# Optimization experiments

Hardware: AMD Instinct MI355X
Metric: run time of the kernel (lower is better)

Reference implementation:

```python
import jax, jax.numpy as jnp
import numpy as np

EPS = 1e-5
CONV_THRESHOLD = 0.0


def setup_inputs() -> dict:
    key = jax.random.key(0)
    ks = jax.random.split(key, 16)
    B, F = 65536, 256
    H1, H2 = 1024, 512
    d_in = F + 1  # raw features + 1 scalar conv feature
    inp = {
        "x": jax.random.normal(ks[0], (B, F), dtype=jnp.float32),
        # layer 1: Linear(d_in, H1) + BatchNorm1d(H1)
        "W1": jax.random.normal(ks[1], (d_in, H1), dtype=jnp.float32) * (1.0 / np.sqrt(d_in)),
        "b1": jax.random.normal(ks[2], (H1,), dtype=jnp.float32) * 0.01,
        "g1": jnp.ones((H1,), jnp.float32) + 0.1 * jax.random.normal(ks[3], (H1,), dtype=jnp.float32),
        "be1": jax.random.normal(ks[4], (H1,), dtype=jnp.float32) * 0.01,
        "m1": jax.random.normal(ks[5], (H1,), dtype=jnp.float32) * 0.1,
        "v1": jax.random.uniform(ks[6], (H1,), dtype=jnp.float32, minval=0.5, maxval=1.5),
        # layer 2: Linear(H1, H2) + BatchNorm1d(H2)
        "W2": jax.random.normal(ks[7], (H1, H2), dtype=jnp.float32) * (1.0 / np.sqrt(H1)),
        "b2": jax.random.normal(ks[8], (H2,), dtype=jnp.float32) * 0.01,
        "g2": jnp.ones((H2,), jnp.float32) + 0.1 * jax.random.normal(ks[9], (H2,), dtype=jnp.float32),
        "be2": jax.random.normal(ks[10], (H2,), dtype=jnp.float32) * 0.01,
        "m2": jax.random.normal(ks[11], (H2,), dtype=jnp.float32) * 0.1,
        "v2": jax.random.uniform(ks[12], (H2,), dtype=jnp.float32, minval=0.5, maxval=1.5),
        # output head: Linear(H2, 1)
        "W3": jax.random.normal(ks[13], (H2, 1), dtype=jnp.float32) * (1.0 / np.sqrt(H2)),
        "b3": jax.random.normal(ks[14], (1,), dtype=jnp.float32) * 0.01,
    }
    return inp


def _bn(h, g, be, m, v):
    # eval-mode BatchNorm1d with running statistics
    return g * (h - m) * jax.lax.rsqrt(v + EPS) + be


def reference(x, W1, b1, g1, be1, m1, v1, W2, b2, g2, be2, m2, v2, W3, b3):
    # Batched replacement of the per-sample numpy threshold conv:
    # the Conv filter reduces the whole sample patch with a mean and thresholds it,
    # producing one binary scalar feature per sample.  [B, 1]
    conv_feat = jnp.where(jnp.mean(x, axis=1, keepdims=True) > CONV_THRESHOLD, 1.0, 0.0).astype(x.dtype)
    h = jnp.concatenate([x, conv_feat], axis=1)  # [B, F+1]
    h = jax.nn.relu(_bn(h @ W1 + b1, g1, be1, m1, v1))  # [B, H1]
    h = jax.nn.relu(_bn(h @ W2 + b2, g2, be2, m2, v2))  # [B, H2]
    return jax.nn.sigmoid(h @ W3 + b3)  # [B, 1]
```

## Files before the change

### kernel.cpp

```cpp
#include <hip/hip_runtime.h>
#include <hip/hip_bf16.h>
#include <cstdint>
#include <cstddef>

typedef __bf16 bf16_t;
typedef bf16_t bf16x8 __attribute__((ext_vector_type(8)));
typedef bf16_t bf16x4 __attribute__((ext_vector_type(4)));
typedef float f32x4 __attribute__((ext_vector_type(4)));

#define BN_EPS 1e-5f

__device__ __forceinline__ void async_load16(const bf16_t* g, bf16_t* lds) {
  __builtin_amdgcn_global_load_lds(
      (__attribute__((address_space(1))) uint32_t*)(g),
      (__attribute__((address_space(3))) uint32_t*)(lds),
      16, 0, 0);
}

__global__ void prep_all_kernel(const float* __restrict__ W1, const float* __restrict__ W2,
                                const float* b1, const float* g1, const float* be1,
                                const float* m1, const float* v1,
                                const float* b2, const float* g2, const float* be2,
                                const float* m2, const float* v2,
                                bf16_t* __restrict__ W1T, bf16_t* __restrict__ W2T,
                                float* s1, float* t1, float* s2, float* t2,
                                float* w1last) {
  const int b = blockIdx.x;
  if (b < 192) {
    const float* src;
    bf16_t* dst;
    int R, C, bx, by;
    if (b < 64) { src = W1; dst = W1T; R = 256; C = 1024; bx = b & 15; by = b >> 4; }
    else        { src = W2; dst = W2T; R = 1024; C = 512; bx = (b - 64) & 7; by = (b - 64) >> 3; }
    __shared__ bf16_t tile[64][66];
    const int r0 = by * 64, c0 = bx * 64;
    const int tc = threadIdx.x & 63;
    const int tr4 = threadIdx.x >> 6;
#pragma unroll
    for (int i = 0; i < 16; ++i) {
      int r = i * 4 + tr4;
      tile[r][tc] = (bf16_t)src[(size_t)(r0 + r) * C + c0 + tc];
    }
    __syncthreads();
#pragma unroll
    for (int i = 0; i < 16; ++i) {
      int rr = i * 4 + tr4;
      dst[(size_t)(c0 + rr) * R + r0 + tc] = tile[tc][rr];
    }
  } else {
    int i = (b - 192) * 256 + threadIdx.x;
    if (i < 1024) {
      float s = g1[i] * rsqrtf(v1[i] + BN_EPS);
      s1[i] = s;
      t1[i] = be1[i] - m1[i] * s + b1[i] * s;
      w1last[i] = W1[256 * 1024 + i];
    }
    if (i < 512) {
      float s = g2[i] * rsqrtf(v2[i] + BN_EPS);
      s2[i] = s;
      t2[i] = be2[i] - m2[i] * s + b2[i] * s;
    }
  }
}

__global__ void prep_x_kernel(const float* __restrict__ x, bf16_t* __restrict__ xb,
                              float* __restrict__ convf, float* __restrict__ outacc) {
  int lane = threadIdx.x & 63;
  int w = threadIdx.x >> 6;
  int row = blockIdx.x * 4 + w;
  const float4 v = *(const float4*)(x + (size_t)row * 256 + lane * 4);
  float s = v.x + v.y + v.z + v.w;
  bf16x4 o = {(bf16_t)v.x, (bf16_t)v.y, (bf16_t)v.z, (bf16_t)v.w};
  *(bf16x4*)(xb + (size_t)row * 256 + lane * 4) = o;
#pragma unroll
  for (int off = 32; off >= 1; off >>= 1) s += __shfl_down(s, off);
  if (lane == 0) convf[row] = (s > 0.0f) ? 1.0f : 0.0f;
  if (threadIdx.x < 4) outacc[blockIdx.x * 4 + threadIdx.x] = 0.0f;
}

__global__ __launch_bounds__(256) void gemm1_kernel(
    const bf16_t* __restrict__ A, const bf16_t* __restrict__ BT,
    const float* __restrict__ sN, const float* __restrict__ tN,
    const float* __restrict__ convf, const float* __restrict__ w1last,
    bf16_t* __restrict__ out) {
  constexpr int K = 256, N = 1024;
  __shared__ __align__(16) bf16_t As[128 * 32];
  __shared__ __align__(16) bf16_t Bs[128 * 32];

  const int tid = threadIdx.x;
  const int lane = tid & 63;
  const int w = tid >> 6;
  const int l15 = lane & 15;
  const int quad = lane >> 4;
  const int wm = (w >> 1) * 64;
  const int wn = (w & 1) * 64;
  const int mTile = blockIdx.y * 128;
  const int nTile = blockIdx.x * 128;

  const int sRow = lane >> 2;
  const int sCol = (lane & 3) * 8;
  const bf16_t* gA = A + (size_t)(mTile + w * 32 + sRow) * K + sCol;
  const bf16_t* gB = BT + (size_t)(nTile + w * 32 + sRow) * K + sCol;
  bf16_t* lA = As + (w * 32) * 32;
  bf16_t* lB = Bs + (w * 32) * 32;

  f32x4 acc[4][4];
#pragma unroll
  for (int i = 0; i < 4; ++i)
#pragma unroll
    for (int j = 0; j < 4; ++j) {
      f32x4 z = {0.f, 0.f, 0.f, 0.f};
      acc[i][j] = z;
    }

  for (int k0 = 0; k0 < K; k0 += 32) {
    async_load16(gA + k0, lA);
    async_load16(gA + (size_t)16 * K + k0, lA + 16 * 32);
    async_load16(gB + k0, lB);
    async_load16(gB + (size_t)16 * K + k0, lB + 16 * 32);
    __syncthreads();

    bf16x8 af[4], bfr[4];
#pragma unroll
    for (int t = 0; t < 4; ++t) {
      af[t] = *(const bf16x8*)(As + (wm + t * 16 + l15) * 32 + quad * 8);
      bfr[t] = *(const bf16x8*)(Bs + (wn + t * 16 + l15) * 32 + quad * 8);
    }
#pragma unroll
    for (int ti = 0; ti < 4; ++ti)
#pragma unroll
      for (int tj = 0; tj < 4; ++tj)
        acc[ti][tj] = __builtin_amdgcn_mfma_f32_16x16x32_bf16(af[ti], bfr[tj], acc[ti][tj], 0, 0, 0);
    __syncthreads();
  }

  float sc[4], tc[4], wl[4];
#pragma unroll
  for (int tj = 0; tj < 4; ++tj) {
    int c = nTile + wn + tj * 16 + l15;
    sc[tj] = sN[c];
    tc[tj] = tN[c];
    wl[tj] = w1last[c];
  }
#pragma unroll
  for (int ti = 0; ti < 4; ++ti)
#pragma unroll
    for (int r = 0; r < 4; ++r) {
      int row = mTile + wm + ti * 16 + quad * 4 + r;
      float cf = convf[row];
      size_t base = (size_t)row * N + nTile + wn;
#pragma unroll
      for (int tj = 0; tj < 4; ++tj) {
        float z = acc[ti][tj][r] + cf * wl[tj];
        z = fmaxf(z * sc[tj] + tc[tj], 0.f);
        out[base + tj * 16 + l15] = (bf16_t)z;
      }
    }
}

__global__ __launch_bounds__(256) void gemm2_head_kernel(
    const bf16_t* __restrict__ A, const bf16_t* __restrict__ BT,
    const float* __restrict__ sN, const float* __restrict__ tN,
    const float* __restrict__ W3, float* __restrict__ outacc) {
  constexpr int K = 1024;
  __shared__ __align__(16) bf16_t As[128 * 32];
  __shared__ __align__(16) bf16_t Bs[128 * 32];
  __shared__ float rowsum[128][2];

  const int b = blockIdx.x;
  const int group = b >> 3;
  const int mTile = (group * 2 + (b & 1)) * 128;
  const int nTile = ((b >> 1) & 3) * 128;

  const int tid = threadIdx.x;
  const int lane = tid & 63;
  const int w = tid >> 6;
  const int l15 = lane & 15;
  const int quad = lane >> 4;
  const int wm = (w >> 1) * 64;
  const int wn = (w & 1) * 64;

  const int sRow = lane >> 2;
  const int sCol = (lane & 3) * 8;
  const bf16_t* gA = A + (size_t)(mTile + w * 32 + sRow) * K + sCol;
  const bf16_t* gB = BT + (size_t)(nTile + w * 32 + sRow) * K + sCol;
  bf16_t* lA = As + (w * 32) * 32;
  bf16_t* lB = Bs + (w * 32) * 32;

  f32x4 acc[4][4];
#pragma unroll
  for (int i = 0; i < 4; ++i)
#pragma unroll
    for (int j = 0; j < 4; ++j) {
      f32x4 z = {0.f, 0.f, 0.f, 0.f};
      acc[i][j] = z;
    }

  for (int k0 = 0; k0 < K; k0 += 32) {
    async_load16(gA + k0, lA);
    async_load16(gA + (size_t)16 * K + k0, lA + 16 * 32);
    async_load16(gB + k0, lB);
    async_load16(gB + (size_t)16 * K + k0, lB + 16 * 32);
    __syncthreads();

    bf16x8 af[4], bfr[4];
#pragma unroll
    for (int t = 0; t < 4; ++t) {
      af[t] = *(const bf16x8*)(As + (wm + t * 16 + l15) * 32 + quad * 8);
      bfr[t] = *(const bf16x8*)(Bs + (wn + t * 16 + l15) * 32 + quad * 8);
    }
#pragma unroll
    for (int ti = 0; ti < 4; ++ti)
#pragma unroll
      for (int tj = 0; tj < 4; ++tj)
        acc[ti][tj] = __builtin_amdgcn_mfma_f32_16x16x32_bf16(af[ti], bfr[tj], acc[ti][tj], 0, 0, 0);
    __syncthreads();
  }

  float sc[4], tc[4], w3c[4];
#pragma unroll
  for (int tj = 0; tj < 4; ++tj) {
    int c = nTile + wn + tj * 16 + l15;
    sc[tj] = sN[c];
    tc[tj] = tN[c];
    w3c[tj] = W3[c];
  }
#pragma unroll
  for (int ti = 0; ti < 4; ++ti)
#pragma unroll
    for (int r = 0; r < 4; ++r) {
      float p = 0.f;
#pragma unroll
      for (int tj = 0; tj < 4; ++tj) {
        float z = fmaxf(acc[ti][tj][r] * sc[tj] + tc[tj], 0.f);
        p += z * w3c[tj];
      }
#pragma unroll
      for (int m = 1; m <= 8; m <<= 1) p += __shfl_xor(p, m);
      if (l15 == 0) rowsum[wm + ti * 16 + quad * 4 + r][wn >> 6] = p;
    }
  __syncthreads();
  if (tid < 128) atomicAdd(outacc + mTile + tid, rowsum[tid][0] + rowsum[tid][1]);
}

__global__ void sigmoid_kernel(float* __restrict__ out, const float* __restrict__ b3) {
  int i = blockIdx.x * 256 + threadIdx.x;
  float z = out[i] + b3[0];
  out[i] = 1.0f / (1.0f + expf(-z));
}

extern "C" void kernel_launch(void* const* d_in, const int* in_sizes, int n_in,
                              void* d_out, int out_size, void* d_ws, size_t ws_size,
                              hipStream_t stream) {
  const float* x = (const float*)d_in[0];
  const float* W1 = (const float*)d_in[1];
  const float* b1 = (const float*)d_in[2];
  const float* g1 = (const float*)d_in[3];
  const float* be1 = (const float*)d_in[4];
  const float* m1 = (const float*)d_in[5];
  const float* v1 = (const float*)d_in[6];
  const float* W2 = (const float*)d_in[7];
  const float* b2 = (const float*)d_in[8];
  const float* g2 = (const float*)d_in[9];
  const float* be2 = (const float*)d_in[10];
  const float* m2 = (const float*)d_in[11];
  const float* v2 = (const float*)d_in[12];
  const float* W3 = (const float*)d_in[13];
  const float* b3 = (const float*)d_in[14];
  float* out = (float*)d_out;

  char* p = (char*)d_ws;
  bf16_t* h1 = (bf16_t*)p;    p += (size_t)65536 * 1024 * 2;
  bf16_t* xb = (bf16_t*)p;    p += (size_t)65536 * 256 * 2;
  bf16_t* W1T = (bf16_t*)p;   p += (size_t)1024 * 256 * 2;
  bf16_t* W2T = (bf16_t*)p;   p += (size_t)512 * 1024 * 2;
  float* convf = (float*)p;   p += (size_t)65536 * 4;
  float* w1last = (float*)p;  p += 1024 * 4;
  float* s1 = (float*)p;      p += 1024 * 4;
  float* t1 = (float*)p;      p += 1024 * 4;
  float* s2 = (float*)p;      p += 512 * 4;
  float* t2 = (float*)p;      p += 512 * 4;

  prep_all_kernel<<<196, 256, 0, stream>>>(W1, W2, b1, g1, be1, m1, v1,
                                           b2, g2, be2, m2, v2,
                                           W1T, W2T, s1, t1, s2, t2, w1last);
  prep_x_kernel<<<16384, 256, 0, stream>>>(x, xb, convf, out);

  gemm1_kernel<<<dim3(8, 512), 256, 0, stream>>>(xb, W1T, s1, t1, convf, w1last, h1);
  gemm2_head_kernel<<<2048, 256, 0, stream>>>(h1, W2T, s2, t2, W3, out);

  sigmoid_kernel<<<256, 256, 0, stream>>>(out, b3);
}
```

Measured before the change: 292.4 us.

## Enlarge GEMM block tiles to 256x128 with 64x128 warp tiles and grouped block order

Both GEMMs move from a 128x128 block tile with 64x64 per-warp subtiles to a 256x128 block tile, where each warp owns a 64x128 strip. Each warp now issues 32 MFMAs per k-step for 4 A and 8 B fragment loads, which raises LDS reuse and halves the number of blocks. Block indices are remapped so groups of 8 M-tiles share N-tiles, for better L2 reuse. The head kernel drops its shared-memory row reduction in favour of direct per-warp atomics, which adds more atomics. The 128 accumulator floats per thread raise register pressure, and launch_bounds(256,2) constrains occupancy.

Result: faster. 256.5 us (-12.3%).

```diff
diff --git a/kernel.cpp b/kernel.cpp
--- a/kernel.cpp
+++ b/kernel.cpp
@@ -78,66 +78,79 @@
   if (threadIdx.x < 4) outacc[blockIdx.x * 4 + threadIdx.x] = 0.0f;
 }
 
-__global__ __launch_bounds__(256) void gemm1_kernel(
+template <int K>
+__device__ __forceinline__ void gemm_core_256x128(
+    const bf16_t* __restrict__ A, const bf16_t* __restrict__ BT,
+    int mTile, int nTile, bf16_t* As, bf16_t* Bs,
+    int w, int lane, f32x4 (&acc)[4][8]) {
+  const int l15 = lane & 15;
+  const int quad = lane >> 4;
+  const int sRow = lane >> 2;
+  const int sCol = (lane & 3) * 8;
+  const bf16_t* gA = A + (size_t)(mTile + w * 64 + sRow) * K + sCol;
+  const bf16_t* gB = BT + (size_t)(nTile + w * 32 + sRow) * K + sCol;
+  bf16_t* lA = As + (w * 64) * 32;
+  bf16_t* lB = Bs + (w * 32) * 32;
+
+  for (int k0 = 0; k0 < K; k0 += 32) {
+    async_load16(gA + k0, lA);
+    async_load16(gA + (size_t)16 * K + k0, lA + 16 * 32);
+    async_load16(gA + (size_t)32 * K + k0, lA + 32 * 32);
+    async_load16(gA + (size_t)48 * K + k0, lA + 48 * 32);
+    async_load16(gB + k0, lB);
+    async_load16(gB + (size_t)16 * K + k0, lB + 16 * 32);
+    __syncthreads();
+
+    bf16x8 af[4], bfr[8];
+#pragma unroll
+    for (int t = 0; t < 4; ++t)
+      af[t] = *(const bf16x8*)(As + (w * 64 + t * 16 + l15) * 32 + quad * 8);
+#pragma unroll
+    for (int t = 0; t < 8; ++t)
+      bfr[t] = *(const bf16x8*)(Bs + (t * 16 + l15) * 32 + quad * 8);
+#pragma unroll
+    for (int ti = 0; ti < 4; ++ti)
+#pragma unroll
+      for (int tj = 0; tj < 8; ++tj)
+        acc[ti][tj] = __builtin_amdgcn_mfma_f32_16x16x32_bf16(af[ti], bfr[tj], acc[ti][tj], 0, 0, 0);
+    __syncthreads();
+  }
+}
+
+__global__ __launch_bounds__(256, 2) void gemm1_kernel(
     const bf16_t* __restrict__ A, const bf16_t* __restrict__ BT,
     const float* __restrict__ sN, const float* __restrict__ tN,
     const float* __restrict__ convf, const float* __restrict__ w1last,
     bf16_t* __restrict__ out) {
   constexpr int K = 256, N = 1024;
-  __shared__ __align__(16) bf16_t As[128 * 32];
+  __shared__ __align__(16) bf16_t As[256 * 32];
   __shared__ __align__(16) bf16_t Bs[128 * 32];
+
+  const int b = blockIdx.x;
+  const int mTile = ((b >> 6) * 8 + (b & 7)) * 256;
+  const int nTile = ((b >> 3) & 7) * 128;
 
   const int tid = threadIdx.x;
   const int lane = tid & 63;
   const int w = tid >> 6;
   const int l15 = lane & 15;
   const int quad = lane >> 4;
-  const int wm = (w >> 1) * 64;
-  const int wn = (w & 1) * 64;
-  const int mTile = blockIdx.y * 128;
-  const int nTile = blockIdx.x * 128;
-
-  const int sRow = lane >> 2;
-  const int sCol = (lane & 3) * 8;
-  const bf16_t* gA = A + (size_t)(mTile + w * 32 + sRow) * K + sCol;
-  const bf16_t* gB = BT + (size_t)(nTile + w * 32 + sRow) * K + sCol;
-  bf16_t* lA = As + (w * 32) * 32;
-  bf16_t* lB = Bs + (w * 32) * 32;
-
-  f32x4 acc[4][4];
+
+  f32x4 acc[4][8];
 #pragma unroll
   for (int i = 0; i < 4; ++i)
 #pragma unroll
-    for (int j = 0; j < 4; ++j) {
+    for (int j = 0; j < 8; ++j) {
       f32x4 z = {0.f, 0.f, 0.f, 0.f};
       acc[i][j] = z;
     }
 
-  for (int k0 = 0; k0 < K; k0 += 32) {
-    async_load16(gA + k0, lA);
-    async_load16(gA + (size_t)16 * K + k0, lA + 16 * 32);
-    async_load16(gB + k0, lB);
-    async_load16(gB + (size_t)16 * K + k0, lB + 16 * 32);
-    __syncthreads();
-
-    bf16x8 af[4], bfr[4];
-#pragma unroll
-    for (int t = 0; t < 4; ++t) {
-      af[t] = *(const bf16x8*)(As + (wm + t * 16 + l15) * 32 + quad * 8);
-      bfr[t] = *(const bf16x8*)(Bs + (wn + t * 16 + l15) * 32 + quad * 8);
-    }
-#pragma unroll
-    for (int ti = 0; ti < 4; ++ti)
-#pragma unroll
-      for (int tj = 0; tj < 4; ++tj)
-        acc[ti][tj] = __builtin_amdgcn_mfma_f32_16x16x32_bf16(af[ti], bfr[tj], acc[ti][tj], 0, 0, 0);
-    __syncthreads();
-  }
-
-  float sc[4], tc[4], wl[4];
-#pragma unroll
-  for (int tj = 0; tj < 4; ++tj) {
-    int c = nTile + wn + tj * 16 + l15;
+  gemm_core_256x128<K>(A, BT, mTile, nTile, As, Bs, w, lane, acc);
+
+  float sc[8], tc[8], wl[8];
+#pragma unroll
+  for (int tj = 0; tj < 8; ++tj) {
+    int c = nTile + tj * 16 + l15;
     sc[tj] = sN[c];
     tc[tj] = tN[c];
     wl[tj] = w1last[c];
@@ -146,11 +159,11 @@
   for (int ti = 0; ti < 4; ++ti)
 #pragma unroll
     for (int r = 0; r < 4; ++r) {
-      int row = mTile + wm + ti * 16 + quad * 4 + r;
+      int row = mTile + w * 64 + ti * 16 + quad * 4 + r;
       float cf = convf[row];
-      size_t base = (size_t)row * N + nTile + wn;
-#pragma unroll
-      for (int tj = 0; tj < 4; ++tj) {
+      size_t base = (size_t)row * N + nTile;
+#pragma unroll
+      for (int tj = 0; tj < 8; ++tj) {
         float z = acc[ti][tj][r] + cf * wl[tj];
         z = fmaxf(z * sc[tj] + tc[tj], 0.f);
         out[base + tj * 16 + l15] = (bf16_t)z;
@@ -158,69 +171,39 @@
     }
 }
 
-__global__ __launch_bounds__(256) void gemm2_head_kernel(
+__global__ __launch_bounds__(256, 2) void gemm2_head_kernel(
     const bf16_t* __restrict__ A, const bf16_t* __restrict__ BT,
     const float* __restrict__ sN, const float* __restrict__ tN,
     const float* __restrict__ W3, float* __restrict__ outacc) {
   constexpr int K = 1024;
-  __shared__ __align__(16) bf16_t As[128 * 32];
+  __shared__ __align__(16) bf16_t As[256 * 32];
   __shared__ __align__(16) bf16_t Bs[128 * 32];
-  __shared__ float rowsum[128][2];
 
   const int b = blockIdx.x;
-  const int group = b >> 3;
-  const int mTile = (group * 2 + (b & 1)) * 128;
-  const int nTile = ((b >> 1) & 3) * 128;
+  const int mTile = ((b >> 5) * 8 + (b & 7)) * 256;
+  const int nTile = ((b >> 3) & 3) * 128;
 
   const int tid = threadIdx.x;
   const int lane = tid & 63;
   const int w = tid >> 6;
   const int l15 = lane & 15;
   const int quad = lane >> 4;
-  const int wm = (w >> 1) * 64;
-  const int wn = (w & 1) * 64;
-
-  const int sRow = lane >> 2;
-  const int sCol = (lane & 3) * 8;
-  const bf16_t* gA = A + (size_t)(mTile + w * 32 + sRow) * K + sCol;
-  const bf16_t* gB = BT + (size_t)(nTile + w * 32 + sRow) * K + sCol;
-  bf16_t* lA = As + (w * 32) * 32;
-  bf16_t* lB = Bs + (w * 32) * 32;
-
-  f32x4 acc[4][4];
+
+  f32x4 acc[4][8];
 #pragma unroll
   for (int i = 0; i < 4; ++i)
 #pragma unroll
-    for (int j = 0; j < 4; ++j) {
+    for (int j = 0; j < 8; ++j) {
       f32x4 z = {0.f, 0.f, 0.f, 0.f};
       acc[i][j] = z;
     }
 
-  for (int k0 = 0; k0 < K; k0 += 32) {
-    async_load16(gA + k0, lA);
-    async_load16(gA + (size_t)16 * K + k0, lA + 16 * 32);
-    async_load16(gB + k0, lB);
-    async_load16(gB + (size_t)16 * K + k0, lB + 16 * 32);
-    __syncthreads();
-
-    bf16x8 af[4], bfr[4];
-#pragma unroll
-    for (int t = 0; t < 4; ++t) {
-      af[t] = *(const bf16x8*)(As + (wm + t * 16 + l15) * 32 + quad * 8);
-      bfr[t] = *(const bf16x8*)(Bs + (wn + t * 16 + l15) * 32 + quad * 8);
-    }
-#pragma unroll
-    for (int ti = 0; ti < 4; ++ti)
-#pragma unroll
-      for (int tj = 0; tj < 4; ++tj)
-        acc[ti][tj] = __builtin_amdgcn_mfma_f32_16x16x32_bf16(af[ti], bfr[tj], acc[ti][tj], 0, 0, 0);
-    __syncthreads();
-  }
-
-  float sc[4], tc[4], w3c[4];
-#pragma unroll
-  for (int tj = 0; tj < 4; ++tj) {
-    int c = nTile + wn + tj * 16 + l15;
+  gemm_core_256x128<K>(A, BT, mTile, nTile, As, Bs, w, lane, acc);
+
+  float sc[8], tc[8], w3c[8];
+#pragma unroll
+  for (int tj = 0; tj < 8; ++tj) {
+    int c = nTile + tj * 16 + l15;
     sc[tj] = sN[c];
     tc[tj] = tN[c];
     w3c[tj] = W3[c];
@@ -231,16 +214,15 @@
     for (int r = 0; r < 4; ++r) {
       float p = 0.f;
 #pragma unroll
-      for (int tj = 0; tj < 4; ++tj) {
+      for (int tj = 0; tj < 8; ++tj) {
         float z = fmaxf(acc[ti][tj][r] * sc[tj] + tc[tj], 0.f);
         p += z * w3c[tj];
       }
 #pragma unroll
       for (int m = 1; m <= 8; m <<= 1) p += __shfl_xor(p, m);
-      if (l15 == 0) rowsum[wm + ti * 16 + quad * 4 + r][wn >> 6] = p;
-    }
-  __syncthreads();
-  if (tid < 128) atomicAdd(outacc + mTile + tid, rowsum[tid][0] + rowsum[tid][1]);
+      if (l15 == 0)
+        atomicAdd(outacc + mTile + w * 64 + ti * 16 + quad * 4 + r, p);
+    }
 }
 
 __global__ void sigmoid_kernel(float* __restrict__ out, const float* __restrict__ b3) {
@@ -286,8 +268,8 @@
                                            W1T, W2T, s1, t1, s2, t2, w1last);
   prep_x_kernel<<<16384, 256, 0, stream>>>(x, xb, convf, out);
 
-  gemm1_kernel<<<dim3(8, 512), 256, 0, stream>>>(xb, W1T, s1, t1, convf, w1last, h1);
-  gemm2_head_kernel<<<2048, 256, 0, stream>>>(h1, W2T, s2, t2, W3, out);
+  gemm1_kernel<<<2048, 256, 0, stream>>>(xb, W1T, s1, t1, convf, w1last, h1);
+  gemm2_head_kernel<<<1024, 256, 0, stream>>>(h1, W2T, s2, t2, W3, out);
 
   sigmoid_kernel<<<256, 256, 0, stream>>>(out, b3);
 }
```
